# Kernel optimization log

Hardware: AMD Instinct MI355X
Metric: run time of the kernel (lower is better)

The kernel has to match this reference:

```python
import jax, jax.numpy as jnp
import numpy as np

EPS = 1e-8

def setup_inputs() -> dict:
    key = jax.random.key(0)
    k1, k2, k3, k4 = jax.random.split(key, 4)
    B, S, D = 64, 512, 512
    emb1 = jax.random.normal(k1, (B, S, D), dtype=jnp.float32)
    emb2 = jax.random.normal(k2, (B, S, D), dtype=jnp.float32)
    # contiguous prefix attention masks (first n tokens valid), as assumed by the original
    len1 = jax.random.randint(k3, (B,), S // 4, S + 1)
    len2 = jax.random.randint(k4, (B,), S // 4, S + 1)
    pos = jnp.arange(S)
    mask1 = (pos[None, :] < len1[:, None]).astype(jnp.int32)
    mask2 = (pos[None, :] < len2[:, None]).astype(jnp.int32)
    return {"article_1_emb": emb1, "article_2_emb": emb2,
            "article_1_att_mask": mask1, "article_2_att_mask": mask2}


def reference(article_1_emb, article_2_emb, article_1_att_mask, article_2_att_mask):
    # L2-normalize token embeddings (cosine similarity = dot of normalized vectors)
    def l2n(x):
        n = jnp.sqrt(jnp.sum(x * x, axis=-1, keepdims=True))
        return x / jnp.maximum(n, EPS)

    e1 = l2n(article_1_emb)   # [B, S1, D]
    e2 = l2n(article_2_emb)   # [B, S2, D]
    sim = jnp.einsum('bid,bjd->bij', e1, e2)  # [B, S1, S2] pairwise cosine sims

    m1 = article_1_att_mask.astype(jnp.bool_)  # [B, S1]
    m2 = article_2_att_mask.astype(jnp.bool_)  # [B, S2]
    NEG = jnp.float32(-1e9)

    # max over valid j for each valid i, and max over valid i for each valid j
    row_max = jnp.max(jnp.where(m2[:, None, :], sim, NEG), axis=2)  # [B, S1]
    col_max = jnp.max(jnp.where(m1[:, :, None], sim, NEG), axis=1)  # [B, S2]
    row_sum = jnp.sum(jnp.where(m1, row_max, 0.0), axis=1)          # [B]
    col_sum = jnp.sum(jnp.where(m2, col_max, 0.0), axis=1)          # [B]

    n1 = jnp.sum(article_1_att_mask, axis=1).astype(jnp.float32)
    n2 = jnp.sum(article_2_att_mask, axis=1).astype(jnp.float32)
    return (row_sum + col_sum) / (n1 + n2)
```

## Files before the change

### kernel.cpp

```cpp
#include <hip/hip_runtime.h>
#include <hip/hip_bf16.h>


typedef __attribute__((ext_vector_type(8))) short bf16x8;
typedef __attribute__((ext_vector_type(4))) float f32x4;

#define NEGBIG (-1e9f)

__device__ __forceinline__ unsigned packbf2_hw(float lo, float hi) {
    __hip_bfloat162 h = __float22bfloat162_rn(float2{lo, hi});
    union { __hip_bfloat162 h; unsigned u; } c; c.h = h;
    return c.u;
}

#define BAR() do {                                            \
        asm volatile("s_waitcnt lgkmcnt(0)" ::: "memory");    \
        __builtin_amdgcn_s_barrier();                         \
        asm volatile("" ::: "memory");                        \
    } while (0)

__global__ __launch_bounds__(256)
void sim_fused(const float* __restrict__ e1, const float* __restrict__ e2,
               const int* __restrict__ m1g, const int* __restrict__ m2g,
               float* __restrict__ rowmax_p,
               float* __restrict__ colmax_p)
{
    const int bid = blockIdx.x;
    const int l   = ((bid & 7) << 7) | (bid >> 3);
    const int b   = l >> 4;
    const int rt  = l & 3;
    const int ct  = (l >> 2) & 3;

    const int tid = threadIdx.x;
    const int lane = tid & 63;
    const int w    = tid >> 6;
    const int wm   = w >> 1;
    const int wn   = w & 1;
    const int q    = lane >> 4;
    const int ln   = lane & 15;
    const int nb   = ct * 128;

    __shared__ __align__(16) ushort sA[2][128 * 32];
    __shared__ __align__(16) ushort sB[2][128 * 32];
    float* spr   = reinterpret_cast<float*>(&sA[0][0]);
    float* spc   = reinterpret_cast<float*>(&sA[0][512]);
    int*   sm1   = reinterpret_cast<int*>(&sA[0][1024]);
    int*   sm2   = reinterpret_cast<int*>(&sA[0][1280]);
    float* sinv1 = reinterpret_cast<float*>(&sB[0][0]);
    float* sinv2 = reinterpret_cast<float*>(&sB[0][256]);

    const int r = tid >> 1;
    const int h = tid & 1;
    const int s = (r ^ (r >> 2)) & 3;
    const float* gA = e1 + ((size_t)(b * 512 + rt * 128 + r)) * 512 + h * 16;
    const float* gB = e2 + ((size_t)(b * 512 + nb + r)) * 512 + h * 16;
    const int wo0 = r * 32 + (((2 * h)     ^ s) << 3);
    const int wo1 = r * 32 + (((2 * h + 1) ^ s) << 3);

    const int sln = (ln & 3) ^ ((ln >> 2) & 3);
    int aoff[4], boff[4];
    #pragma unroll
    for (int mt = 0; mt < 4; ++mt)
        aoff[mt] = (wm * 64 + mt * 16 + ln) * 32 + ((q ^ sln) << 3);
    #pragma unroll
    for (int nt = 0; nt < 4; ++nt)
        boff[nt] = (wn * 64 + nt * 16 + ln) * 32 + ((q ^ sln) << 3);

    float ssA = 0.f, ssB = 0.f;
    float4 ra[2][4], rb[2][4];

    auto LOADK = [&](int u, int kf) {
        const float4* pa = reinterpret_cast<const float4*>(gA + kf);
        const float4* pb = reinterpret_cast<const float4*>(gB + kf);
        ra[u][0] = pa[0]; ra[u][1] = pa[1]; ra[u][2] = pa[2]; ra[u][3] = pa[3];
        rb[u][0] = pb[0]; rb[u][1] = pb[1]; rb[u][2] = pb[2]; rb[u][3] = pb[3];
    };
    auto CVTWRITE = [&](int u, int pd) {
        #pragma unroll
        for (int i = 0; i < 4; ++i) {
            ssA += ra[u][i].x * ra[u][i].x + ra[u][i].y * ra[u][i].y
                 + ra[u][i].z * ra[u][i].z + ra[u][i].w * ra[u][i].w;
            ssB += rb[u][i].x * rb[u][i].x + rb[u][i].y * rb[u][i].y
                 + rb[u][i].z * rb[u][i].z + rb[u][i].w * rb[u][i].w;
        }
        uint4 v;
        v.x = packbf2_hw(ra[u][0].x, ra[u][0].y); v.y = packbf2_hw(ra[u][0].z, ra[u][0].w);
        v.z = packbf2_hw(ra[u][1].x, ra[u][1].y); v.w = packbf2_hw(ra[u][1].z, ra[u][1].w);
        *reinterpret_cast<uint4*>(&sA[pd][wo0]) = v;
        v.x = packbf2_hw(ra[u][2].x, ra[u][2].y); v.y = packbf2_hw(ra[u][2].z, ra[u][2].w);
        v.z = packbf2_hw(ra[u][3].x, ra[u][3].y); v.w = packbf2_hw(ra[u][3].z, ra[u][3].w);
        *reinterpret_cast<uint4*>(&sA[pd][wo1]) = v;
        v.x = packbf2_hw(rb[u][0].x, rb[u][0].y); v.y = packbf2_hw(rb[u][0].z, rb[u][0].w);
        v.z = packbf2_hw(rb[u][1].x, rb[u][1].y); v.w = packbf2_hw(rb[u][1].z, rb[u][1].w);
        *reinterpret_cast<uint4*>(&sB[pd][wo0]) = v;
        v.x = packbf2_hw(rb[u][2].x, rb[u][2].y); v.y = packbf2_hw(rb[u][2].z, rb[u][2].w);
        v.z = packbf2_hw(rb[u][3].x, rb[u][3].y); v.w = packbf2_hw(rb[u][3].z, rb[u][3].w);
        *reinterpret_cast<uint4*>(&sB[pd][wo1]) = v;
    };

    f32x4 acc[4][4];
    #pragma unroll
    for (int i = 0; i < 4; ++i)
        #pragma unroll
        for (int j = 0; j < 4; ++j)
            acc[i][j] = (f32x4){0.f, 0.f, 0.f, 0.f};

    LOADK(0, 0);
    CVTWRITE(0, 0);
    LOADK(1, 32);
    BAR();

#define HALF_ITER(P, K)                                                    \
    do {                                                                   \
        if ((K) < 14) LOADK(P, ((K) + 2) * 32);                            \
        bf16x8 af[4], bfr[4];                                              \
        _Pragma("unroll")                                                  \
        for (int mt = 0; mt < 4; ++mt)                                     \
            af[mt] = *reinterpret_cast<const bf16x8*>(&sA[P][aoff[mt]]);   \
        _Pragma("unroll")                                                  \
        for (int nt = 0; nt < 4; ++nt)                                     \
            bfr[nt] = *reinterpret_cast<const bf16x8*>(&sB[P][boff[nt]]);  \
        if ((K) < 15) CVTWRITE((P) ^ 1, (P) ^ 1);                          \
        _Pragma("unroll")                                                  \
        for (int mt = 0; mt < 4; ++mt)                                     \
            _Pragma("unroll")                                              \
            for (int nt = 0; nt < 4; ++nt)                                 \
                acc[mt][nt] = __builtin_amdgcn_mfma_f32_16x16x32_bf16(     \
                    af[mt], bfr[nt], acc[mt][nt], 0, 0, 0);                \
        BAR();                                                             \
    } while (0)

    for (int kk = 0; kk < 8; ++kk) {
        HALF_ITER(0, 2 * kk);
        HALF_ITER(1, 2 * kk + 1);
    }
#undef HALF_ITER

    if (tid < 128) sm1[tid] = m1g[b * 512 + rt * 128 + tid];
    else           sm2[tid - 128] = m2g[b * 512 + nb + (tid - 128)];
    ssA += __shfl_xor(ssA, 1);
    ssB += __shfl_xor(ssB, 1);
    if (h == 0) {
        sinv1[r] = 1.0f / fmaxf(sqrtf(ssA), 1e-8f);
        sinv2[r] = 1.0f / fmaxf(sqrtf(ssB), 1e-8f);
    }
    BAR();

    float invj[4];
    f32x4 invi[4];
    #pragma unroll
    for (int nt = 0; nt < 4; ++nt)
        invj[nt] = sinv2[wn * 64 + nt * 16 + ln];
    #pragma unroll
    for (int mt = 0; mt < 4; ++mt)
        #pragma unroll
        for (int rg = 0; rg < 4; ++rg)
            invi[mt][rg] = sinv1[wm * 64 + mt * 16 + q * 4 + rg];
    #pragma unroll
    for (int mt = 0; mt < 4; ++mt)
        #pragma unroll
        for (int nt = 0; nt < 4; ++nt)
            acc[mt][nt] = acc[mt][nt] * (invi[mt] * invj[nt]);

    #pragma unroll
    for (int mt = 0; mt < 4; ++mt) {
        #pragma unroll
        for (int rg = 0; rg < 4; ++rg) {
            float rm = NEGBIG;
            #pragma unroll
            for (int nt = 0; nt < 4; ++nt) {
                float v = sm2[wn * 64 + nt * 16 + ln] ? acc[mt][nt][rg] : NEGBIG;
                rm = fmaxf(rm, v);
            }
            rm = fmaxf(rm, __shfl_xor(rm, 1));
            rm = fmaxf(rm, __shfl_xor(rm, 2));
            rm = fmaxf(rm, __shfl_xor(rm, 4));
            rm = fmaxf(rm, __shfl_xor(rm, 8));
            if (ln == 0) spr[wn * 128 + wm * 64 + mt * 16 + q * 4 + rg] = rm;
        }
    }
    #pragma unroll
    for (int nt = 0; nt < 4; ++nt) {
        float cm = NEGBIG;
        #pragma unroll
        for (int mt = 0; mt < 4; ++mt)
            #pragma unroll
            for (int rg = 0; rg < 4; ++rg) {
                float v = sm1[wm * 64 + mt * 16 + q * 4 + rg] ? acc[mt][nt][rg] : NEGBIG;
                cm = fmaxf(cm, v);
            }
        cm = fmaxf(cm, __shfl_xor(cm, 16));
        cm = fmaxf(cm, __shfl_xor(cm, 32));
        if (lane < 16) spc[wm * 128 + wn * 64 + nt * 16 + ln] = cm;
    }
    BAR();
    if (tid < 128) {
        rowmax_p[((size_t)b * 4 + ct) * 512 + rt * 128 + tid] =
            fmaxf(spr[tid], spr[128 + tid]);
        colmax_p[((size_t)b * 4 + rt) * 512 + nb + tid] =
            fmaxf(spc[tid], spc[128 + tid]);
    }
}

__global__ __launch_bounds__(256)
void final_kernel(const int* __restrict__ m1g, const int* __restrict__ m2g,
                  const float* __restrict__ rowmax_p, const float* __restrict__ colmax_p,
                  float* __restrict__ out)
{
    const int b = blockIdx.x;
    const int tid = threadIdx.x;
    const int lane = tid & 63;
    const int w = tid >> 6;

    float sum = 0.f;
    float nn  = 0.f;
    for (int j = tid; j < 512; j += 256) {
        int mm1 = m1g[b * 512 + j];
        int mm2 = m2g[b * 512 + j];
        nn += (float)(mm1 + mm2);
        const float* rp = rowmax_p + (size_t)b * 2048 + j;
        float rm = fmaxf(fmaxf(rp[0], rp[512]), fmaxf(rp[1024], rp[1536]));
        if (mm1) sum += rm;
        const float* cp = colmax_p + (size_t)b * 2048 + j;
        float cm = fmaxf(fmaxf(cp[0], cp[512]), fmaxf(cp[1024], cp[1536]));
        if (mm2) sum += cm;
    }
    #pragma unroll
    for (int m = 32; m; m >>= 1) {
        sum += __shfl_xor(sum, m);
        nn  += __shfl_xor(nn, m);
    }
    __shared__ float ssum[4], snn[4];
    if (lane == 0) { ssum[w] = sum; snn[w] = nn; }
    __syncthreads();
    if (tid == 0) {
        float S = ssum[0] + ssum[1] + ssum[2] + ssum[3];
        float N = snn[0] + snn[1] + snn[2] + snn[3];
        out[b] = S / N;
    }
}

extern "C" void kernel_launch(void* const* d_in, const int* in_sizes, int n_in,
                              void* d_out, int out_size, void* d_ws, size_t ws_size,
                              hipStream_t stream) {
    const float* e1 = (const float*)d_in[0];
    const float* e2 = (const float*)d_in[1];
    const int*   m1 = (const int*)d_in[2];
    const int*   m2 = (const int*)d_in[3];
    float* out = (float*)d_out;

    float* ws = (float*)d_ws;
    float* rowmax_p = ws;
    float* colmax_p = ws + 131072;

    sim_fused<<<dim3(1024), 256, 0, stream>>>(e1, e2, m1, m2,
                                              rowmax_p, colmax_p);
    final_kernel<<<64, 256, 0, stream>>>(m1, m2, rowmax_p, colmax_p, out);
}
```

Before: 177.2 us.

## Double block to 512 threads, splitting A and B staging across thread halves

Each block now runs 8 waves instead of 4. The first 256 threads load and convert the e1 tile and the second 256 load the e2 tile, so each thread stages half the data it did before. Each wave computes a 64x32 output sub-tile instead of 64x64, and the row-max reduction combines four partial slots. The goal is to hide global-load latency for this memory-bound kernel with more waves in flight and fewer registers per thread, at the cost of extra barrier participants and less MFMA work per LDS fragment load.

```diff
diff --git a/kernel.cpp b/kernel.cpp
--- a/kernel.cpp
+++ b/kernel.cpp
@@ -19,7 +19,7 @@
         asm volatile("" ::: "memory");                        \
     } while (0)
 
-__global__ __launch_bounds__(256)
+__global__ __launch_bounds__(512)
 void sim_fused(const float* __restrict__ e1, const float* __restrict__ e2,
                const int* __restrict__ m1g, const int* __restrict__ m2g,
                float* __restrict__ rowmax_p,
@@ -31,11 +31,11 @@
     const int rt  = l & 3;
     const int ct  = (l >> 2) & 3;
 
-    const int tid = threadIdx.x;
+    const int tid  = threadIdx.x;
     const int lane = tid & 63;
     const int w    = tid >> 6;
-    const int wm   = w >> 1;
-    const int wn   = w & 1;
+    const int wm   = w >> 2;
+    const int wn   = w & 3;
     const int q    = lane >> 4;
     const int ln   = lane & 15;
     const int nb   = ct * 128;
@@ -43,88 +43,83 @@
     __shared__ __align__(16) ushort sA[2][128 * 32];
     __shared__ __align__(16) ushort sB[2][128 * 32];
     float* spr   = reinterpret_cast<float*>(&sA[0][0]);
-    float* spc   = reinterpret_cast<float*>(&sA[0][512]);
-    int*   sm1   = reinterpret_cast<int*>(&sA[0][1024]);
-    int*   sm2   = reinterpret_cast<int*>(&sA[0][1280]);
+    float* spc   = reinterpret_cast<float*>(&sA[0][1024]);
+    int*   sm1   = reinterpret_cast<int*>(&sA[0][1536]);
+    int*   sm2   = reinterpret_cast<int*>(&sA[0][1792]);
     float* sinv1 = reinterpret_cast<float*>(&sB[0][0]);
     float* sinv2 = reinterpret_cast<float*>(&sB[0][256]);
 
-    const int r = tid >> 1;
-    const int h = tid & 1;
-    const int s = (r ^ (r >> 2)) & 3;
-    const float* gA = e1 + ((size_t)(b * 512 + rt * 128 + r)) * 512 + h * 16;
-    const float* gB = e2 + ((size_t)(b * 512 + nb + r)) * 512 + h * 16;
+    const int  tt  = tid & 255;
+    const int  r   = tt >> 1;
+    const int  h   = tt & 1;
+    const int  s   = (r ^ (r >> 2)) & 3;
+    const bool isA = (tid < 256);
+    const float* gsrc = (isA
+        ? e1 + ((size_t)(b * 512 + rt * 128 + r)) * 512
+        : e2 + ((size_t)(b * 512 + nb + r)) * 512) + h * 16;
+    ushort* const wb0 = isA ? &sA[0][0] : &sB[0][0];
+    ushort* const wb1 = isA ? &sA[1][0] : &sB[1][0];
     const int wo0 = r * 32 + (((2 * h)     ^ s) << 3);
     const int wo1 = r * 32 + (((2 * h + 1) ^ s) << 3);
 
     const int sln = (ln & 3) ^ ((ln >> 2) & 3);
-    int aoff[4], boff[4];
+    int aoff[4], boff[2];
     #pragma unroll
     for (int mt = 0; mt < 4; ++mt)
         aoff[mt] = (wm * 64 + mt * 16 + ln) * 32 + ((q ^ sln) << 3);
     #pragma unroll
-    for (int nt = 0; nt < 4; ++nt)
-        boff[nt] = (wn * 64 + nt * 16 + ln) * 32 + ((q ^ sln) << 3);
-
-    float ssA = 0.f, ssB = 0.f;
-    float4 ra[2][4], rb[2][4];
+    for (int nt = 0; nt < 2; ++nt)
+        boff[nt] = (wn * 32 + nt * 16 + ln) * 32 + ((q ^ sln) << 3);
+
+    float ss = 0.f;
+    float4 rg_[2][4];
 
     auto LOADK = [&](int u, int kf) {
-        const float4* pa = reinterpret_cast<const float4*>(gA + kf);
-        const float4* pb = reinterpret_cast<const float4*>(gB + kf);
-        ra[u][0] = pa[0]; ra[u][1] = pa[1]; ra[u][2] = pa[2]; ra[u][3] = pa[3];
-        rb[u][0] = pb[0]; rb[u][1] = pb[1]; rb[u][2] = pb[2]; rb[u][3] = pb[3];
+        const float4* p = reinterpret_cast<const float4*>(gsrc + kf);
+        rg_[u][0] = p[0]; rg_[u][1] = p[1]; rg_[u][2] = p[2]; rg_[u][3] = p[3];
     };
-    auto CVTWRITE = [&](int u, int pd) {
+    auto CVTWRITE = [&](int u, ushort* wb) {
         #pragma unroll
         for (int i = 0; i < 4; ++i) {
-            ssA += ra[u][i].x * ra[u][i].x + ra[u][i].y * ra[u][i].y
-                 + ra[u][i].z * ra[u][i].z + ra[u][i].w * ra[u][i].w;
-            ssB += rb[u][i].x * rb[u][i].x + rb[u][i].y * rb[u][i].y
-                 + rb[u][i].z * rb[u][i].z + rb[u][i].w * rb[u][i].w;
+            ss += rg_[u][i].x * rg_[u][i].x + rg_[u][i].y * rg_[u][i].y
+                + rg_[u][i].z * rg_[u][i].z + rg_[u][i].w * rg_[u][i].w;
         }
         uint4 v;
-        v.x = packbf2_hw(ra[u][0].x, ra[u][0].y); v.y = packbf2_hw(ra[u][0].z, ra[u][0].w);
-        v.z = packbf2_hw(ra[u][1].x, ra[u][1].y); v.w = packbf2_hw(ra[u][1].z, ra[u][1].w);
-        *reinterpret_cast<uint4*>(&sA[pd][wo0]) = v;
-        v.x = packbf2_hw(ra[u][2].x, ra[u][2].y); v.y = packbf2_hw(ra[u][2].z, ra[u][2].w);
-        v.z = packbf2_hw(ra[u][3].x, ra[u][3].y); v.w = packbf2_hw(ra[u][3].z, ra[u][3].w);
-        *reinterpret_cast<uint4*>(&sA[pd][wo1]) = v;
-        v.x = packbf2_hw(rb[u][0].x, rb[u][0].y); v.y = packbf2_hw(rb[u][0].z, rb[u][0].w);
-        v.z = packbf2_hw(rb[u][1].x, rb[u][1].y); v.w = packbf2_hw(rb[u][1].z, rb[u][1].w);
-        *reinterpret_cast<uint4*>(&sB[pd][wo0]) = v;
-        v.x = packbf2_hw(rb[u][2].x, rb[u][2].y); v.y = packbf2_hw(rb[u][2].z, rb[u][2].w);
-        v.z = packbf2_hw(rb[u][3].x, rb[u][3].y); v.w = packbf2_hw(rb[u][3].z, rb[u][3].w);
-        *reinterpret_cast<uint4*>(&sB[pd][wo1]) = v;
+        v.x = packbf2_hw(rg_[u][0].x, rg_[u][0].y); v.y = packbf2_hw(rg_[u][0].z, rg_[u][0].w);
+        v.z = packbf2_hw(rg_[u][1].x, rg_[u][1].y); v.w = packbf2_hw(rg_[u][1].z, rg_[u][1].w);
+        *reinterpret_cast<uint4*>(wb + wo0) = v;
+        v.x = packbf2_hw(rg_[u][2].x, rg_[u][2].y); v.y = packbf2_hw(rg_[u][2].z, rg_[u][2].w);
+        v.z = packbf2_hw(rg_[u][3].x, rg_[u][3].y); v.w = packbf2_hw(rg_[u][3].z, rg_[u][3].w);
+        *reinterpret_cast<uint4*>(wb + wo1) = v;
     };
 
-    f32x4 acc[4][4];
+    f32x4 acc[4][2];
     #pragma unroll
     for (int i = 0; i < 4; ++i)
         #pragma unroll
-        for (int j = 0; j < 4; ++j)
+        for (int j = 0; j < 2; ++j)
             acc[i][j] = (f32x4){0.f, 0.f, 0.f, 0.f};
 
     LOADK(0, 0);
-    CVTWRITE(0, 0);
+    CVTWRITE(0, wb0);
     LOADK(1, 32);
     BAR();
 
 #define HALF_ITER(P, K)                                                    \
     do {                                                                   \
         if ((K) < 14) LOADK(P, ((K) + 2) * 32);                            \
-        bf16x8 af[4], bfr[4];                                              \
+        bf16x8 af[4], bfr[2];                                              \
         _Pragma("unroll")                                                  \
         for (int mt = 0; mt < 4; ++mt)                                     \
             af[mt] = *reinterpret_cast<const bf16x8*>(&sA[P][aoff[mt]]);   \
         _Pragma("unroll")                                                  \
-        for (int nt = 0; nt < 4; ++nt)                                     \
+        for (int nt = 0; nt < 2; ++nt)                                     \
             bfr[nt] = *reinterpret_cast<const bf16x8*>(&sB[P][boff[nt]]);  \
-        if ((K) < 15) CVTWRITE((P) ^ 1, (P) ^ 1);                          \
+        if ((K) < 15) CVTWRITE((P) ^ 1, ((P) ^ 1) ? wb1 : wb0);            \
         _Pragma("unroll")                                                  \
         for (int mt = 0; mt < 4; ++mt)                                     \
             _Pragma("unroll")                                              \
-            for (int nt = 0; nt < 4; ++nt)                                 \
+            for (int nt = 0; nt < 2; ++nt)                                 \
                 acc[mt][nt] = __builtin_amdgcn_mfma_f32_16x16x32_bf16(     \
                     af[mt], bfr[nt], acc[mt][nt], 0, 0, 0);                \
         BAR();                                                             \
@@ -136,21 +131,21 @@
     }
 #undef HALF_ITER
 
-    if (tid < 128) sm1[tid] = m1g[b * 512 + rt * 128 + tid];
-    else           sm2[tid - 128] = m2g[b * 512 + nb + (tid - 128)];
-    ssA += __shfl_xor(ssA, 1);
-    ssB += __shfl_xor(ssB, 1);
+    if (tid < 128)      sm1[tid]       = m1g[b * 512 + rt * 128 + tid];
+    else if (tid < 256) sm2[tid - 128] = m2g[b * 512 + nb + (tid - 128)];
+    ss += __shfl_xor(ss, 1);
     if (h == 0) {
-        sinv1[r] = 1.0f / fmaxf(sqrtf(ssA), 1e-8f);
-        sinv2[r] = 1.0f / fmaxf(sqrtf(ssB), 1e-8f);
+        float inv = 1.0f / fmaxf(sqrtf(ss), 1e-8f);
+        if (isA) sinv1[r] = inv;
+        else     sinv2[r] = inv;
     }
     BAR();
 
-    float invj[4];
+    float invj[2];
     f32x4 invi[4];
     #pragma unroll
-    for (int nt = 0; nt < 4; ++nt)
-        invj[nt] = sinv2[wn * 64 + nt * 16 + ln];
+    for (int nt = 0; nt < 2; ++nt)
+        invj[nt] = sinv2[wn * 32 + nt * 16 + ln];
     #pragma unroll
     for (int mt = 0; mt < 4; ++mt)
         #pragma unroll
@@ -159,7 +154,7 @@
     #pragma unroll
     for (int mt = 0; mt < 4; ++mt)
         #pragma unroll
-        for (int nt = 0; nt < 4; ++nt)
+        for (int nt = 0; nt < 2; ++nt)
             acc[mt][nt] = acc[mt][nt] * (invi[mt] * invj[nt]);
 
     #pragma unroll
@@ -168,8 +163,8 @@
         for (int rg = 0; rg < 4; ++rg) {
             float rm = NEGBIG;
             #pragma unroll
-            for (int nt = 0; nt < 4; ++nt) {
-                float v = sm2[wn * 64 + nt * 16 + ln] ? acc[mt][nt][rg] : NEGBIG;
+            for (int nt = 0; nt < 2; ++nt) {
+                float v = sm2[wn * 32 + nt * 16 + ln] ? acc[mt][nt][rg] : NEGBIG;
                 rm = fmaxf(rm, v);
             }
             rm = fmaxf(rm, __shfl_xor(rm, 1));
@@ -180,7 +175,7 @@
         }
     }
     #pragma unroll
-    for (int nt = 0; nt < 4; ++nt) {
+    for (int nt = 0; nt < 2; ++nt) {
         float cm = NEGBIG;
         #pragma unroll
         for (int mt = 0; mt < 4; ++mt)
@@ -191,12 +186,13 @@
             }
         cm = fmaxf(cm, __shfl_xor(cm, 16));
         cm = fmaxf(cm, __shfl_xor(cm, 32));
-        if (lane < 16) spc[wm * 128 + wn * 64 + nt * 16 + ln] = cm;
+        if (lane < 16) spc[wm * 128 + wn * 32 + nt * 16 + ln] = cm;
     }
     BAR();
     if (tid < 128) {
         rowmax_p[((size_t)b * 4 + ct) * 512 + rt * 128 + tid] =
-            fmaxf(spr[tid], spr[128 + tid]);
+            fmaxf(fmaxf(spr[tid], spr[128 + tid]),
+                  fmaxf(spr[256 + tid], spr[384 + tid]));
         colmax_p[((size_t)b * 4 + rt) * 512 + nb + tid] =
             fmaxf(spc[tid], spc[128 + tid]);
     }
@@ -253,7 +249,7 @@
     float* rowmax_p = ws;
     float* colmax_p = ws + 131072;
 
-    sim_fused<<<dim3(1024), 256, 0, stream>>>(e1, e2, m1, m2,
+    sim_fused<<<dim3(1024), 512, 0, stream>>>(e1, e2, m1, m2,
                                               rowmax_p, colmax_p);
     final_kernel<<<64, 256, 0, stream>>>(m1, m2, rowmax_p, colmax_p, out);
 }
```

After: 178.7 us. No clear change (+0.8%).

## Split into normalize-to-bf16 prep kernel and direct-to-LDS bf16 MFMA GEMM

Applied to the files above, without the earlier changes.

Adds a prep kernel that L2-normalizes each row once and writes it to workspace as bf16 in a swizzled layout. A new GEMM kernel then streams those bf16 tiles into LDS with global_load_lds, double-buffered, and runs MFMA plus the masked row/col max epilogue. This removes the repeated fp32 load, normalize and convert work that the fused kernel did per tile, and halves the bytes the GEMM reads. In exchange it writes and re-reads a 64 MB bf16 copy through workspace and adds a launch. If the workspace is too small it falls back to the old fused kernel.

```diff
diff --git a/kernel.cpp b/kernel.cpp
--- a/kernel.cpp
+++ b/kernel.cpp
@@ -19,11 +19,192 @@
         asm volatile("" ::: "memory");                        \
     } while (0)
 
+#define BARV() do {                                           \
+        asm volatile("s_waitcnt vmcnt(0)" ::: "memory");      \
+        __builtin_amdgcn_s_barrier();                         \
+        asm volatile("" ::: "memory");                        \
+    } while (0)
+
+__device__ __forceinline__ void glds16(const ushort* g, ushort* l) {
+    __builtin_amdgcn_global_load_lds(
+        (const __attribute__((address_space(1))) unsigned int*)(const void*)g,
+        (__attribute__((address_space(3))) unsigned int*)(void*)l,
+        16, 0, 0);
+}
+
 __global__ __launch_bounds__(256)
-void sim_fused(const float* __restrict__ e1, const float* __restrict__ e2,
-               const int* __restrict__ m1g, const int* __restrict__ m2g,
-               float* __restrict__ rowmax_p,
-               float* __restrict__ colmax_p)
+void prep_kernel(const float* __restrict__ e1, const float* __restrict__ e2,
+                 ushort* __restrict__ e1n, ushort* __restrict__ e2n)
+{
+    const int bid = blockIdx.x;
+    const int l   = ((bid & 7) << 7) | (bid >> 3);
+    const int b   = l >> 4;
+    const int idx = l & 15;
+    const int lane = threadIdx.x & 63;
+    const int w    = threadIdx.x >> 6;
+    const float*  src = (idx < 8) ? e1 : e2;
+    ushort*       dst = (idx < 8) ? e1n : e2n;
+    const int rbase = (idx & 7) * 64;
+
+    #pragma unroll 4
+    for (int i = 0; i < 16; ++i) {
+        const int row = rbase + w * 16 + i;
+        const size_t off = ((size_t)b * 512 + row) * 512;
+        const float4* p = reinterpret_cast<const float4*>(src + off) + lane * 2;
+        float4 x = p[0], y = p[1];
+        float ss = x.x*x.x + x.y*x.y + x.z*x.z + x.w*x.w
+                 + y.x*y.x + y.y*y.y + y.z*y.z + y.w*y.w;
+        #pragma unroll
+        for (int m = 1; m < 64; m <<= 1) ss += __shfl_xor(ss, m);
+        const float inv = 1.0f / fmaxf(sqrtf(ss), 1e-8f);
+        x.x *= inv; x.y *= inv; x.z *= inv; x.w *= inv;
+        y.x *= inv; y.y *= inv; y.z *= inv; y.w *= inv;
+        uint4 v;
+        v.x = packbf2_hw(x.x, x.y); v.y = packbf2_hw(x.z, x.w);
+        v.z = packbf2_hw(y.x, y.y); v.w = packbf2_hw(y.z, y.w);
+        const int s = (row ^ (row >> 2)) & 3;
+        *reinterpret_cast<uint4*>(dst + off + (lane >> 2) * 32
+                                  + ((lane & 3) ^ s) * 8) = v;
+    }
+}
+
+__global__ __launch_bounds__(256)
+void sim_gemm(const ushort* __restrict__ e1n, const ushort* __restrict__ e2n,
+              const int* __restrict__ m1g, const int* __restrict__ m2g,
+              float* __restrict__ rowmax_p, float* __restrict__ colmax_p)
+{
+    const int bid = blockIdx.x;
+    const int l   = ((bid & 7) << 7) | (bid >> 3);
+    const int b   = l >> 4;
+    const int rt  = l & 3;
+    const int ct  = (l >> 2) & 3;
+
+    const int tid  = threadIdx.x;
+    const int lane = tid & 63;
+    const int w    = tid >> 6;
+    const int wm   = w >> 1;
+    const int wn   = w & 1;
+    const int q    = lane >> 4;
+    const int ln   = lane & 15;
+    const int nb   = ct * 128;
+
+    __shared__ __align__(16) ushort sA[2][128 * 32];
+    __shared__ __align__(16) ushort sB[2][128 * 32];
+    float* spr = reinterpret_cast<float*>(&sA[0][0]);
+    float* spc = reinterpret_cast<float*>(&sA[0][512]);
+    int*   sm1 = reinterpret_cast<int*>(&sA[0][1024]);
+    int*   sm2 = reinterpret_cast<int*>(&sA[0][1280]);
+
+    const int rs = lane >> 2;
+    const int ks = (lane & 3) * 8;
+    const ushort* gA0 = e1n + ((size_t)(b * 512 + rt * 128 + 2 * w * 16 + rs)) * 512 + ks;
+    const ushort* gA1 = gA0 + 16 * 512;
+    const ushort* gB0 = e2n + ((size_t)(b * 512 + nb + 2 * w * 16 + rs)) * 512 + ks;
+    const ushort* gB1 = gB0 + 16 * 512;
+    const int dch = w * 1024;
+
+    const int sln = (ln & 3) ^ ((ln >> 2) & 3);
+    int aoff[4], boff[4];
+    #pragma unroll
+    for (int mt = 0; mt < 4; ++mt)
+        aoff[mt] = (wm * 64 + mt * 16 + ln) * 32 + ((q ^ sln) << 3);
+    #pragma unroll
+    for (int nt = 0; nt < 4; ++nt)
+        boff[nt] = (wn * 64 + nt * 16 + ln) * 32 + ((q ^ sln) << 3);
+
+    f32x4 acc[4][4];
+    #pragma unroll
+    for (int i = 0; i < 4; ++i)
+        #pragma unroll
+        for (int j = 0; j < 4; ++j)
+            acc[i][j] = (f32x4){0.f, 0.f, 0.f, 0.f};
+
+#define STAGE(P2, KT)                                                       \
+    do {                                                                    \
+        const int k32 = (KT) * 32;                                          \
+        glds16(gA0 + k32, &sA[P2][dch]);                                    \
+        glds16(gA1 + k32, &sA[P2][dch + 512]);                              \
+        glds16(gB0 + k32, &sB[P2][dch]);                                    \
+        glds16(gB1 + k32, &sB[P2][dch + 512]);                              \
+    } while (0)
+
+    STAGE(0, 0);
+    BARV();
+
+#define ITER(P, K)                                                          \
+    do {                                                                    \
+        if ((K) < 15) STAGE((P) ^ 1, (K) + 1);                              \
+        bf16x8 af[4], bfr[4];                                               \
+        _Pragma("unroll")                                                   \
+        for (int mt = 0; mt < 4; ++mt)                                      \
+            af[mt] = *reinterpret_cast<const bf16x8*>(&sA[P][aoff[mt]]);    \
+        _Pragma("unroll")                                                   \
+        for (int nt = 0; nt < 4; ++nt)                                      \
+            bfr[nt] = *reinterpret_cast<const bf16x8*>(&sB[P][boff[nt]]);   \
+        _Pragma("unroll")                                                   \
+        for (int mt = 0; mt < 4; ++mt)                                      \
+            _Pragma("unroll")                                               \
+            for (int nt = 0; nt < 4; ++nt)                                  \
+                acc[mt][nt] = __builtin_amdgcn_mfma_f32_16x16x32_bf16(      \
+                    af[mt], bfr[nt], acc[mt][nt], 0, 0, 0);                 \
+        BARV();                                                             \
+    } while (0)
+
+    for (int kk = 0; kk < 8; ++kk) {
+        ITER(0, 2 * kk);
+        ITER(1, 2 * kk + 1);
+    }
+#undef ITER
+#undef STAGE
+
+    if (tid < 128) sm1[tid] = m1g[b * 512 + rt * 128 + tid];
+    else           sm2[tid - 128] = m2g[b * 512 + nb + (tid - 128)];
+    BAR();
+
+    #pragma unroll
+    for (int mt = 0; mt < 4; ++mt) {
+        #pragma unroll
+        for (int rg = 0; rg < 4; ++rg) {
+            float rm = NEGBIG;
+            #pragma unroll
+            for (int nt = 0; nt < 4; ++nt) {
+                float v = sm2[wn * 64 + nt * 16 + ln] ? acc[mt][nt][rg] : NEGBIG;
+                rm = fmaxf(rm, v);
+            }
+            rm = fmaxf(rm, __shfl_xor(rm, 1));
+            rm = fmaxf(rm, __shfl_xor(rm, 2));
+            rm = fmaxf(rm, __shfl_xor(rm, 4));
+            rm = fmaxf(rm, __shfl_xor(rm, 8));
+            if (ln == 0) spr[wn * 128 + wm * 64 + mt * 16 + q * 4 + rg] = rm;
+        }
+    }
+    #pragma unroll
+    for (int nt = 0; nt < 4; ++nt) {
+        float cm = NEGBIG;
+        #pragma unroll
+        for (int mt = 0; mt < 4; ++mt)
+            #pragma unroll
+            for (int rg = 0; rg < 4; ++rg) {
+                float v = sm1[wm * 64 + mt * 16 + q * 4 + rg] ? acc[mt][nt][rg] : NEGBIG;
+                cm = fmaxf(cm, v);
+            }
+        cm = fmaxf(cm, __shfl_xor(cm, 16));
+        cm = fmaxf(cm, __shfl_xor(cm, 32));
+        if (lane < 16) spc[wm * 128 + wn * 64 + nt * 16 + ln] = cm;
+    }
+    BAR();
+    if (tid < 128) {
+        rowmax_p[((size_t)b * 4 + ct) * 512 + rt * 128 + tid] =
+            fmaxf(spr[tid], spr[128 + tid]);
+        colmax_p[((size_t)b * 4 + rt) * 512 + nb + tid] =
+            fmaxf(spc[tid], spc[128 + tid]);
+    }
+}
+
+__global__ __launch_bounds__(256)
+void sim_fused_fb(const float* __restrict__ e1, const float* __restrict__ e2,
+                  const int* __restrict__ m1g, const int* __restrict__ m2g,
+                  float* __restrict__ rowmax_p, float* __restrict__ colmax_p)
 {
     const int bid = blockIdx.x;
     const int l   = ((bid & 7) << 7) | (bid >> 3);
@@ -253,7 +434,18 @@
     float* rowmax_p = ws;
     float* colmax_p = ws + 131072;
 
-    sim_fused<<<dim3(1024), 256, 0, stream>>>(e1, e2, m1, m2,
-                                              rowmax_p, colmax_p);
+    const size_t PANEL = (size_t)64 * 512 * 512;
+    const size_t NEED  = 1048576 + 2 * PANEL * sizeof(ushort);
+
+    if (ws_size >= NEED) {
+        ushort* e1n = (ushort*)((char*)d_ws + 1048576);
+        ushort* e2n = e1n + PANEL;
+        prep_kernel<<<dim3(1024), 256, 0, stream>>>(e1, e2, e1n, e2n);
+        sim_gemm<<<dim3(1024), 256, 0, stream>>>(e1n, e2n, m1, m2,
+                                                 rowmax_p, colmax_p);
+    } else {
+        sim_fused_fb<<<dim3(1024), 256, 0, stream>>>(e1, e2, m1, m2,
+                                                     rowmax_p, colmax_p);
+    }
     final_kernel<<<64, 256, 0, stream>>>(m1, m2, rowmax_p, colmax_p, out);
 }
```

Measured after the change: 193.9 us. 9.4% more time.
